# Performance work log

Measured on AMD Instinct MI355X. Metric: run time of the kernel, lower is better.

## Reference

```python
import jax, jax.numpy as jnp
import numpy as np

H = 1024  # hidden_size


def _lstm_layer(x, w_ih, w_hh, b_ih, b_hh):
    # x: [S, B, I] -> outputs [S, B, H]
    S, B, _ = x.shape
    # Precompute input projection for all timesteps (both biases folded in,
    # matching gi + gh where gi carries b_ih and gh carries b_hh).
    gi = jnp.einsum('sbi,gi->sbg', x, w_ih) + b_ih + b_hh  # [S, B, 4H]
    h0 = jnp.zeros((B, H), x.dtype)
    c0 = jnp.zeros((B, H), x.dtype)

    def step(carry, gi_t):
        h, c = carry
        gates = gi_t + h @ w_hh.T                # [B, 4H]
        i, f, g, o = jnp.split(gates, 4, axis=1)  # gate order: i, f, g, o
        c_new = jax.nn.sigmoid(f) * c + jax.nn.sigmoid(i) * jnp.tanh(g)
        h_new = jax.nn.sigmoid(o) * jnp.tanh(c_new)
        return (h_new, c_new), h_new

    (h_last, c_last), ys = jax.lax.scan(step, (h0, c0), gi)
    return ys, h_last, c_last


def setup_inputs() -> dict:
    key = jax.random.key(0)
    ks = jax.random.split(key, 6)
    S, B, I = 512, 64, 1024
    def xavier(k, shape):
        fan_out, fan_in = shape
        lim = np.sqrt(6.0 / (fan_in + fan_out)).astype(np.float32)
        return jax.random.uniform(k, shape, jnp.float32, -lim, lim)
    return {
        'x': jax.random.normal(ks[0], (S, B, I), jnp.float32),
        'w_ih_0': xavier(ks[1], (4 * H, I)),
        'w_hh_0': xavier(ks[2], (4 * H, H)),
        'b_ih_0': jnp.zeros((4 * H,), jnp.float32),
        'b_hh_0': jnp.zeros((4 * H,), jnp.float32),
        'w_ih_1': xavier(ks[3], (4 * H, H)),
        'w_hh_1': xavier(ks[4], (4 * H, H)),
        'b_ih_1': jnp.zeros((4 * H,), jnp.float32),
        'b_hh_1': jnp.zeros((4 * H,), jnp.float32),
    }


def reference(x, w_ih_0, w_hh_0, b_ih_0, b_hh_0, w_ih_1, w_hh_1, b_ih_1, b_hh_1):
    # 2-layer unidirectional LSTM, dropout=0, batch_first=False, zero init state.
    y0, h0, c0 = _lstm_layer(x, w_ih_0, w_hh_0, b_ih_0, b_hh_0)
    y1, h1, c1 = _lstm_layer(y0, w_ih_1, w_hh_1, b_ih_1, b_hh_1)
    h_n = jnp.stack([h0, h1], axis=0)  # [num_layers, B, H]
    c_n = jnp.stack([c0, c1], axis=0)
    return y1, h_n, c_n
```

## Files before the change

### kernel.cpp

```cpp
#include <hip/hip_runtime.h>

typedef __attribute__((ext_vector_type(8))) short short8;
typedef __attribute__((ext_vector_type(4))) float f32x4;
typedef unsigned int uint32;
typedef unsigned long long u64;

#define OFF_GI    0ull
#define OFF_XB    268435456ull
#define OFF_WIH0  335544320ull
#define OFF_WPKI  343932928ull
#define OFF_WPK0  352321536ull
#define OFF_WPK1  360710144ull
#define OFF_B0    369098752ull
#define OFF_B1    369115136ull
#define OFF_CNT   369131520ull
#define OFF_HBUF  369164288ull
#define WS_REQUIRED 369426432ull

#define ALOAD(p)    __hip_atomic_load((p), __ATOMIC_RELAXED, __HIP_MEMORY_SCOPE_AGENT)
#define ASTOREV(p,v) __hip_atomic_store((p), (v), __ATOMIC_RELAXED, __HIP_MEMORY_SCOPE_AGENT)
#define AADD(p,v)   __hip_atomic_fetch_add((p), (v), __ATOMIC_RELAXED, __HIP_MEMORY_SCOPE_AGENT)
#define WD_ITERS 30000

__device__ __forceinline__ unsigned short f2bf(float f) {
    union { float f; uint32 u; } v; v.f = f;
    uint32 u = v.u + 0x7FFFu + ((v.u >> 16) & 1u);
    return (unsigned short)(u >> 16);
}
__device__ __forceinline__ float bf2f(unsigned short u) {
    union { uint32 u; float f; } v; v.u = ((uint32)u) << 16; return v.f;
}
__device__ __forceinline__ float sigmoidf_(float x) {
    return 1.0f / (1.0f + __expf(-x));
}
__device__ __forceinline__ float tanhf_(float x) {
    return 1.0f - 2.0f / (1.0f + __expf(2.0f * x));
}

__global__ void diag_kernel(float* out, float val) {
    if (blockIdx.x == 0 && threadIdx.x == 0) out[0] = val;
}

__global__ void cast_bf16_kernel(const float* __restrict__ in,
                                 unsigned short* __restrict__ out, int n4) {
    int i = blockIdx.x * 256 + threadIdx.x;
    if (i < n4) {
        float4 v = ((const float4*)in)[i];
        ushort4 o;
        o.x = f2bf(v.x); o.y = f2bf(v.y); o.z = f2bf(v.z); o.w = f2bf(v.w);
        ((ushort4*)out)[i] = o;
    }
}

__global__ void bias_sum_kernel(const float* __restrict__ a,
                                const float* __restrict__ b,
                                float* __restrict__ o, int n) {
    int i = blockIdx.x * 256 + threadIdx.x;
    if (i < n) o[i] = a[i] + b[i];
}

__global__ void bias_perm_kernel(const float* __restrict__ a,
                                 const float* __restrict__ b,
                                 float* __restrict__ o) {
    int i = blockIdx.x * 256 + threadIdx.x;
    int c = i >> 2, g = i & 3;
    o[i] = a[g * 1024 + c] + b[g * 1024 + c];
}

__global__ void pack_whh_kernel(const float* __restrict__ whh,
                                unsigned short* __restrict__ out) {
    int o = blockIdx.x * 256 + threadIdx.x;
    int j  = o & 7;
    int l  = (o >> 3) & 63;
    int f  = (o >> 9) & 31;
    int wq = o >> 14;
    int w = wq >> 2, q = wq & 3;
    int g = f >> 3,  s = f & 7;
    int n = g * 1024 + w * 16 + (l & 15);
    int k = q * 256 + s * 32 + ((l >> 4)) * 8 + j;
    out[o] = f2bf(whh[(size_t)n * 1024 + k]);
}

__global__ void pack_wih1_frag_kernel(const float* __restrict__ wih1,
                                      unsigned short* __restrict__ out) {
    int o = blockIdx.x * 256 + threadIdx.x;
    int j  = o & 7;
    int l  = (o >> 3) & 63;
    int ks = (o >> 9) & 31;
    int wq = o >> 14;
    int w = wq >> 2, q = wq & 3;
    int np = w * 64 + q * 16 + (l & 15);
    int c = np >> 2, g = np & 3;
    int k = ks * 32 + ((l >> 4)) * 8 + j;
    out[o] = f2bf(wih1[(size_t)(g * 1024 + c) * 1024 + k]);
}

__global__ __launch_bounds__(256, 2) void gemm_bt_kernel(
    const unsigned short* __restrict__ A,
    const unsigned short* __restrict__ B,
    const float* __restrict__ bias,
    unsigned short* __restrict__ C) {
    __shared__ __align__(16) unsigned short As[128 * 64];
    __shared__ __align__(16) unsigned short Bs[128 * 64];
    const int tid = threadIdx.x;
    const int l = tid & 63;
    const int wv = tid >> 6;
    const int wm = wv >> 1, wn = wv & 1;
    const long bm = blockIdx.x, bn = blockIdx.y;

    f32x4 acc[4][4];
#pragma unroll
    for (int i = 0; i < 4; ++i)
#pragma unroll
        for (int j = 0; j < 4; ++j)
            acc[i][j] = (f32x4){0.f, 0.f, 0.f, 0.f};

    for (int k0 = 0; k0 < 1024; k0 += 64) {
#pragma unroll
        for (int ii = 0; ii < 4; ++ii) {
            int slot = ii * 256 + tid;
            int row = slot >> 3, csw = slot & 7;
            int cc = csw ^ (row & 7);
            *(uint4*)&As[slot * 8] =
                *(const uint4*)(A + (bm * 128 + row) * 1024 + k0 + cc * 8);
            *(uint4*)&Bs[slot * 8] =
                *(const uint4*)(B + (bn * 128 + row) * 1024 + k0 + cc * 8);
        }
        __syncthreads();
#pragma unroll
        for (int s = 0; s < 2; ++s) {
            short8 af[4], bfm[4];
#pragma unroll
            for (int i = 0; i < 4; ++i) {
                int row = wm * 64 + i * 16 + (l & 15);
                af[i] = *(const short8*)&As[(row * 8 + (((s * 4) + (l >> 4)) ^ (row & 7))) * 8];
            }
#pragma unroll
            for (int j = 0; j < 4; ++j) {
                int row = wn * 64 + j * 16 + (l & 15);
                bfm[j] = *(const short8*)&Bs[(row * 8 + (((s * 4) + (l >> 4)) ^ (row & 7))) * 8];
            }
#pragma unroll
            for (int i = 0; i < 4; ++i)
#pragma unroll
                for (int j = 0; j < 4; ++j)
                    acc[i][j] = __builtin_amdgcn_mfma_f32_16x16x32_bf16(
                        af[i], bfm[j], acc[i][j], 0, 0, 0);
        }
        __syncthreads();
    }
#pragma unroll
    for (int j = 0; j < 4; ++j) {
        float bj = bias[bn * 128 + wn * 64 + j * 16 + (l & 15)];
#pragma unroll
        for (int i = 0; i < 4; ++i) {
#pragma unroll
            for (int r = 0; r < 4; ++r) {
                long row = bm * 128 + wm * 64 + i * 16 + (l >> 4) * 4 + r;
                C[row * 4096 + bn * 128 + wn * 64 + j * 16 + (l & 15)] =
                    f2bf(acc[i][j][r] + bj);
            }
        }
    }
}

__device__ __forceinline__ void gi1_tile(
    const unsigned short* hs,
    const unsigned short* __restrict__ wpkI,
    const float* __restrict__ b1p,
    unsigned short* gi1,
    int tg, int p, int w, int q, int l)
{
    f32x4 gacc = (f32x4){0.f, 0.f, 0.f, 0.f};
    const int arow = l & 15;
    const unsigned short* wb = wpkI + (size_t)(w * 4 + q) * 16384 + (size_t)l * 8;
#pragma unroll 4
    for (int ks = 0; ks < 32; ++ks) {
        short8 bfk = *(const short8*)(wb + ks * 512);
        short8 afk = *(const short8*)&hs[(arow * 128 + ((ks * 4 + (l >> 4)) ^ (arow & 7))) * 8];
        gacc = __builtin_amdgcn_mfma_f32_16x16x32_bf16(afk, bfk, gacc, 0, 0, 0);
    }
    const int colp = w * 64 + q * 16 + (l & 15);
    float bj = b1p[colp];
#pragma unroll
    for (int r = 0; r < 4; ++r) {
        int v0 = f2bf(gacc[r] + bj);
        int v1 = __shfl_down(v0, 1);
        int v2 = __shfl_down(v0, 2);
        int v3 = __shfl_down(v0, 3);
        if ((l & 3) == 0) {
            size_t row = (size_t)tg * 64 + p * 16 + (l >> 4) * 4 + r;
            u64 u = (u64)(v0 & 0xffff) | ((u64)(v1 & 0xffff) << 16) |
                    ((u64)(v2 & 0xffff) << 32) | ((u64)(v3 & 0xffff) << 48);
            *(u64*)(gi1 + row * 4096 + colp) = u;
        }
    }
}

__global__ __launch_bounds__(256, 2) void lstm_l0_fused_kernel(
    unsigned short* gi,
    const unsigned short* __restrict__ wpk0,
    const unsigned short* __restrict__ wpkI,
    const float* __restrict__ b1p,
    unsigned short* hbuf,
    float* __restrict__ hn, float* __restrict__ cn,
    int* cnt)
{
    __shared__ __align__(16) char smem[49152];
    const int bid = blockIdx.x;
    const int tid = threadIdx.x;
    const int l = tid & 63, q = tid >> 6;

    if (bid < 256) {
        unsigned short* hs = (unsigned short*)smem;
        float (*red)[4][16][16] = (float (*)[4][16][16])(smem + 32768);
        const int p = bid >> 6, w = bid & 63;
        int* cg = cnt + p * 2048;
        int* pr = cnt + p * 2048 + 1024;

        short8 bfr[4][8];
        {
            const unsigned short* wb = wpk0 + (size_t)((w * 4 + q) * 32) * 512 + (size_t)l * 8;
#pragma unroll
            for (int g = 0; g < 4; ++g)
#pragma unroll
                for (int s = 0; s < 8; ++s)
                    bfr[g][s] = *(const short8*)(wb + (g * 8 + s) * 512);
        }

        float c_state = 0.0f;
        const int be = tid >> 4, je = tid & 15;
        const int hrow = p * 16 + be;
        const int hcol = w * 16 + je;

        for (int t = 0; t < 512; ++t) {
            const unsigned short* gp = gi + (size_t)t * 262144 + (size_t)hrow * 4096 + hcol;
            float g0 = bf2f(gp[0]);
            float g1 = bf2f(gp[1024]);
            float g2 = bf2f(gp[2048]);
            float g3 = bf2f(gp[3072]);

            if (tid == 0) {
                if (t > 0) {
                    int iters = 0;
                    while (ALOAD(&cg[t - 1]) < 64) {
                        __builtin_amdgcn_s_sleep(2);
                        if (++iters > WD_ITERS) break;
                    }
                }
                if (t >= 2) {
                    int iters = 0;
                    while (ALOAD(&pr[t - 2]) < 64) {
                        __builtin_amdgcn_s_sleep(2);
                        if (++iters > WD_ITERS) break;
                    }
                }
            }
            __syncthreads();

            {
                const u64* hp64 = (const u64*)(hbuf + (size_t)(t & 1) * 65536);
#pragma unroll
                for (int ii = 0; ii < 8; ++ii) {
                    int slot = ii * 256 + tid;
                    int row = slot >> 7, cs = slot & 127;
                    int cc = cs ^ (row & 7);
                    size_t gidx = ((size_t)(p * 16 + row) * 1024 + (size_t)cc * 8) >> 2;
                    u64 lo = ALOAD(&hp64[gidx]);
                    u64 hi = ALOAD(&hp64[gidx + 1]);
                    *(u64*)&hs[slot * 8]     = lo;
                    *(u64*)&hs[slot * 8 + 4] = hi;
                }
            }
            __syncthreads();

            f32x4 acc[4];
#pragma unroll
            for (int g = 0; g < 4; ++g) acc[g] = (f32x4){0.f, 0.f, 0.f, 0.f};
            const int arow = l & 15;
#pragma unroll
            for (int s = 0; s < 8; ++s) {
                int chunk = q * 32 + s * 4 + (l >> 4);
                short8 af = *(const short8*)&hs[(arow * 128 + (chunk ^ (arow & 7))) * 8];
#pragma unroll
                for (int g = 0; g < 4; ++g)
                    acc[g] = __builtin_amdgcn_mfma_f32_16x16x32_bf16(
                        af, bfr[g][s], acc[g], 0, 0, 0);
            }
#pragma unroll
            for (int g = 0; g < 4; ++g)
#pragma unroll
                for (int r = 0; r < 4; ++r)
                    red[q][g][(l >> 4) * 4 + r][l & 15] = acc[g][r];
            __syncthreads();

            float gate_i = g0, gate_f = g1, gate_g = g2, gate_o = g3;
#pragma unroll
            for (int qq = 0; qq < 4; ++qq) {
                gate_i += red[qq][0][be][je];
                gate_f += red[qq][1][be][je];
                gate_g += red[qq][2][be][je];
                gate_o += red[qq][3][be][je];
            }
            float ig = sigmoidf_(gate_i);
            float fg = sigmoidf_(gate_f);
            float gg = tanhf_(gate_g);
            float og = sigmoidf_(gate_o);
            c_state = fg * c_state + ig * gg;
            float h_new = og * tanhf_(c_state);

            unsigned short hb = f2bf(h_new);
            {
                int v0 = hb;
                int v1 = __shfl_down(v0, 1);
                int v2 = __shfl_down(v0, 2);
                int v3 = __shfl_down(v0, 3);
                if ((l & 3) == 0) {
                    u64 u = (u64)(v0 & 0xffff) | ((u64)(v1 & 0xffff) << 16) |
                            ((u64)(v2 & 0xffff) << 32) | ((u64)(v3 & 0xffff) << 48);
                    u64* dst = (u64*)(hbuf + (size_t)((t + 1) & 1) * 65536 +
                                      (size_t)hrow * 1024 + hcol);
                    ASTOREV(dst, u);
                }
            }
            if (t == 511) {
                hn[(size_t)hrow * 1024 + hcol] = h_new;
                cn[(size_t)hrow * 1024 + hcol] = c_state;
            }
            __syncthreads();
            if (tid == 0) AADD(&cg[t], 1);
        }
    } else {
        unsigned short* hs = (unsigned short*)smem;
        const int W = bid - 256;
        const int p = W >> 6, w = W & 63;
        int* cg = cnt + p * 2048;
        int* pr = cnt + p * 2048 + 1024;

        for (int t = 0; t < 512; ++t) {
            if (tid == 0) {
                int iters = 0;
                while (ALOAD(&cg[t]) < 64) {
                    __builtin_amdgcn_s_sleep(2);
                    if (++iters > WD_ITERS) break;
                }
            }
            __syncthreads();

            {
                const u64* hp64 = (const u64*)(hbuf + (size_t)((t + 1) & 1) * 65536);
#pragma unroll
                for (int ii = 0; ii < 8; ++ii) {
                    int slot = ii * 256 + tid;
                    int row = slot >> 7, cs = slot & 127;
                    int cc = cs ^ (row & 7);
                    size_t gidx = ((size_t)(p * 16 + row) * 1024 + (size_t)cc * 8) >> 2;
                    u64 lo = ALOAD(&hp64[gidx]);
                    u64 hi = ALOAD(&hp64[gidx + 1]);
                    *(u64*)&hs[slot * 8]     = lo;
                    *(u64*)&hs[slot * 8 + 4] = hi;
                }
            }
            __syncthreads();
            if (tid == 0) AADD(&pr[t], 1);

            gi1_tile(hs, wpkI, b1p, gi, t, p, w, q, l);
        }
    }
}

__global__ __launch_bounds__(256, 2) void lstm_rec1_kernel(
    const unsigned short* __restrict__ gi,
    const unsigned short* __restrict__ wpk,
    unsigned short* hbuf,
    float* __restrict__ yf,
    float* __restrict__ hn, float* __restrict__ cn,
    int* cnt) {
    __shared__ __align__(16) unsigned short hs[16 * 1024];
    __shared__ float red[4][4][16][16];
    const int tid = threadIdx.x;
    const int l = tid & 63, q = tid >> 6;
    const int W = blockIdx.x;
    const int p = W >> 6, w = W & 63;
    int* cg = cnt + p * 2048;

    short8 bfr[4][8];
    {
        const unsigned short* wb = wpk + (size_t)((w * 4 + q) * 32) * 512 + (size_t)l * 8;
#pragma unroll
        for (int g = 0; g < 4; ++g)
#pragma unroll
            for (int s = 0; s < 8; ++s)
                bfr[g][s] = *(const short8*)(wb + (g * 8 + s) * 512);
    }

    float c_state = 0.0f;
    const int be = tid >> 4, je = tid & 15;
    const int hrow = p * 16 + be;
    const int hcol = w * 16 + je;

    for (int t = 0; t < 512; ++t) {
        u64 gv = *(const u64*)(gi + ((size_t)t * 64 + hrow) * 4096 + (size_t)hcol * 4);
        float g0 = bf2f((unsigned short)gv);
        float g1 = bf2f((unsigned short)(gv >> 16));
        float g2 = bf2f((unsigned short)(gv >> 32));
        float g3 = bf2f((unsigned short)(gv >> 48));

        if (t > 0 && tid == 0) {
            int iters = 0;
            while (ALOAD(&cg[t - 1]) < 64) {
                __builtin_amdgcn_s_sleep(2);
                if (++iters > WD_ITERS) break;
            }
        }
        __syncthreads();

        {
            const u64* hp64 = (const u64*)(hbuf + (size_t)(t & 1) * 65536);
#pragma unroll
            for (int ii = 0; ii < 8; ++ii) {
                int slot = ii * 256 + tid;
                int row = slot >> 7, cs = slot & 127;
                int cc = cs ^ (row & 7);
                size_t gidx = ((size_t)(p * 16 + row) * 1024 + (size_t)cc * 8) >> 2;
                u64 lo = ALOAD(&hp64[gidx]);
                u64 hi = ALOAD(&hp64[gidx + 1]);
                *(u64*)&hs[slot * 8]     = lo;
                *(u64*)&hs[slot * 8 + 4] = hi;
            }
        }
        __syncthreads();

        f32x4 acc[4];
#pragma unroll
        for (int g = 0; g < 4; ++g) acc[g] = (f32x4){0.f, 0.f, 0.f, 0.f};
        const int arow = l & 15;
#pragma unroll
        for (int s = 0; s < 8; ++s) {
            int chunk = q * 32 + s * 4 + (l >> 4);
            short8 af = *(const short8*)&hs[(arow * 128 + (chunk ^ (arow & 7))) * 8];
#pragma unroll
            for (int g = 0; g < 4; ++g)
                acc[g] = __builtin_amdgcn_mfma_f32_16x16x32_bf16(
                    af, bfr[g][s], acc[g], 0, 0, 0);
        }
#pragma unroll
        for (int g = 0; g < 4; ++g)
#pragma unroll
            for (int r = 0; r < 4; ++r)
                red[q][g][(l >> 4) * 4 + r][l & 15] = acc[g][r];
        __syncthreads();

        float gate_i = g0, gate_f = g1, gate_g = g2, gate_o = g3;
#pragma unroll
        for (int qq = 0; qq < 4; ++qq) {
            gate_i += red[qq][0][be][je];
            gate_f += red[qq][1][be][je];
            gate_g += red[qq][2][be][je];
            gate_o += red[qq][3][be][je];
        }
        float ig = sigmoidf_(gate_i);
        float fg = sigmoidf_(gate_f);
        float gg = tanhf_(gate_g);
        float og = sigmoidf_(gate_o);
        c_state = fg * c_state + ig * gg;
        float h_new = og * tanhf_(c_state);

        unsigned short hb = f2bf(h_new);
        {
            int v0 = hb;
            int v1 = __shfl_down(v0, 1);
            int v2 = __shfl_down(v0, 2);
            int v3 = __shfl_down(v0, 3);
            if ((l & 3) == 0) {
                u64 u = (u64)(v0 & 0xffff) | ((u64)(v1 & 0xffff) << 16) |
                        ((u64)(v2 & 0xffff) << 32) | ((u64)(v3 & 0xffff) << 48);
                u64* dst = (u64*)(hbuf + (size_t)((t + 1) & 1) * 65536 +
                                  (size_t)hrow * 1024 + hcol);
                ASTOREV(dst, u);
            }
        }
        yf[(size_t)t * 65536 + (size_t)hrow * 1024 + hcol] = h_new;
        if (t == 511) {
            hn[(size_t)hrow * 1024 + hcol] = h_new;
            cn[(size_t)hrow * 1024 + hcol] = c_state;
        }
        __syncthreads();
        if (tid == 0) AADD(&cg[t], 1);
    }
}

extern "C" void kernel_launch(void* const* d_in, const int* in_sizes, int n_in,
                              void* d_out, int out_size, void* d_ws, size_t ws_size,
                              hipStream_t stream) {
    const float* x    = (const float*)d_in[0];
    const float* wih0 = (const float*)d_in[1];
    const float* whh0 = (const float*)d_in[2];
    const float* bih0 = (const float*)d_in[3];
    const float* bhh0 = (const float*)d_in[4];
    const float* wih1 = (const float*)d_in[5];
    const float* whh1 = (const float*)d_in[6];
    const float* bih1 = (const float*)d_in[7];
    const float* bhh1 = (const float*)d_in[8];
    float* out = (float*)d_out;

    if (ws_size < WS_REQUIRED) {
        diag_kernel<<<1, 64, 0, stream>>>(out, (float)(ws_size >> 20));
        return;
    }

    char* ws = (char*)d_ws;
    unsigned short* gi    = (unsigned short*)(ws + OFF_GI);
    unsigned short* xb    = (unsigned short*)(ws + OFF_XB);
    unsigned short* wih0b = (unsigned short*)(ws + OFF_WIH0);
    unsigned short* wpkI  = (unsigned short*)(ws + OFF_WPKI);
    unsigned short* wpk0  = (unsigned short*)(ws + OFF_WPK0);
    unsigned short* wpk1  = (unsigned short*)(ws + OFF_WPK1);
    float*          b0    = (float*)(ws + OFF_B0);
    float*          b1p   = (float*)(ws + OFF_B1);
    int*            cnt   = (int*)(ws + OFF_CNT);
    unsigned short* hbuf  = (unsigned short*)(ws + OFF_HBUF);

    cast_bf16_kernel<<<32768, 256, 0, stream>>>(x, xb, 8388608);
    cast_bf16_kernel<<<4096, 256, 0, stream>>>(wih0, wih0b, 1048576);
    pack_wih1_frag_kernel<<<16384, 256, 0, stream>>>(wih1, wpkI);
    pack_whh_kernel<<<16384, 256, 0, stream>>>(whh0, wpk0);
    pack_whh_kernel<<<16384, 256, 0, stream>>>(whh1, wpk1);
    bias_sum_kernel<<<16, 256, 0, stream>>>(bih0, bhh0, b0, 4096);
    bias_perm_kernel<<<16, 256, 0, stream>>>(bih1, bhh1, b1p);

    gemm_bt_kernel<<<dim3(256, 32), 256, 0, stream>>>(xb, wih0b, b0, gi);

    hipMemsetAsync(cnt, 0, 32768 + 262144, stream);
    lstm_l0_fused_kernel<<<512, 256, 0, stream>>>(gi, wpk0, wpkI, b1p, hbuf,
                                                  out + 33554432, out + 33685504,
                                                  cnt);
    hipMemsetAsync(cnt, 0, 32768 + 262144, stream);
    lstm_rec1_kernel<<<256, 256, 0, stream>>>(gi, wpk1, hbuf, out,
                                              out + 33554432 + 65536,
                                              out + 33685504 + 65536,
                                              cnt);
}
```

Measured before the change: 5.998 ms.

## Run both LSTM layers concurrently in one persistent kernel with wavefront pipelining

Merges the layer-0 recurrence, the layer-1 input projection and the layer-1 recurrence into a single persistent kernel. Blocks 0-255 run layer 0 while blocks 256-511 run layer 1 a few steps behind, exchanging h through an 8-slot ring buffer guarded by per-step counters. The x-to-bf16 cast is also folded into the GEMM's A-tile load, which removes a separate pass over x. This trades two serialized 512-step recurrences for one pipelined schedule, at the cost of more cross-block synchronization and more shared memory per block. Layer 1 now computes its input projection for step t+1 on its own critical path.

```diff
diff --git a/kernel.cpp b/kernel.cpp
--- a/kernel.cpp
+++ b/kernel.cpp
@@ -6,15 +6,15 @@
 typedef unsigned long long u64;
 
 #define OFF_GI    0ull
-#define OFF_XB    268435456ull
+#define OFF_Y0R   268435456ull
+#define OFF_H1B   269484032ull
+#define OFF_CNT2  269746176ull
 #define OFF_WIH0  335544320ull
 #define OFF_WPKI  343932928ull
 #define OFF_WPK0  352321536ull
 #define OFF_WPK1  360710144ull
 #define OFF_B0    369098752ull
 #define OFF_B1    369115136ull
-#define OFF_CNT   369131520ull
-#define OFF_HBUF  369164288ull
 #define WS_REQUIRED 369426432ull
 
 #define ALOAD(p)    __hip_atomic_load((p), __ATOMIC_RELAXED, __HIP_MEMORY_SCOPE_AGENT)
@@ -95,8 +95,8 @@
     out[o] = f2bf(wih1[(size_t)(g * 1024 + c) * 1024 + k]);
 }
 
-__global__ __launch_bounds__(256, 2) void gemm_bt_kernel(
-    const unsigned short* __restrict__ A,
+__global__ __launch_bounds__(256, 2) void gemm_bt_f32a_kernel(
+    const float* __restrict__ A,
     const unsigned short* __restrict__ B,
     const float* __restrict__ bias,
     unsigned short* __restrict__ C) {
@@ -121,8 +121,14 @@
             int slot = ii * 256 + tid;
             int row = slot >> 3, csw = slot & 7;
             int cc = csw ^ (row & 7);
-            *(uint4*)&As[slot * 8] =
-                *(const uint4*)(A + (bm * 128 + row) * 1024 + k0 + cc * 8);
+            const float* ap = A + (size_t)(bm * 128 + row) * 1024 + k0 + cc * 8;
+            float4 va = ((const float4*)ap)[0];
+            float4 vb = ((const float4*)ap)[1];
+            ushort4 ua, ub;
+            ua.x = f2bf(va.x); ua.y = f2bf(va.y); ua.z = f2bf(va.z); ua.w = f2bf(va.w);
+            ub.x = f2bf(vb.x); ub.y = f2bf(vb.y); ub.z = f2bf(vb.z); ub.w = f2bf(vb.w);
+            *(ushort4*)&As[slot * 8]     = ua;
+            *(ushort4*)&As[slot * 8 + 4] = ub;
             *(uint4*)&Bs[slot * 8] =
                 *(const uint4*)(B + (bn * 128 + row) * 1024 + k0 + cc * 8);
         }
@@ -164,60 +170,34 @@
     }
 }
 
-__device__ __forceinline__ void gi1_tile(
-    const unsigned short* hs,
+__global__ __launch_bounds__(256, 2) void lstm_fused2_kernel(
+    const unsigned short* __restrict__ gi0,
+    const unsigned short* __restrict__ wpk0,
+    const unsigned short* __restrict__ wpk1,
     const unsigned short* __restrict__ wpkI,
     const float* __restrict__ b1p,
-    unsigned short* gi1,
-    int tg, int p, int w, int q, int l)
-{
-    f32x4 gacc = (f32x4){0.f, 0.f, 0.f, 0.f};
-    const int arow = l & 15;
-    const unsigned short* wb = wpkI + (size_t)(w * 4 + q) * 16384 + (size_t)l * 8;
-#pragma unroll 4
-    for (int ks = 0; ks < 32; ++ks) {
-        short8 bfk = *(const short8*)(wb + ks * 512);
-        short8 afk = *(const short8*)&hs[(arow * 128 + ((ks * 4 + (l >> 4)) ^ (arow & 7))) * 8];
-        gacc = __builtin_amdgcn_mfma_f32_16x16x32_bf16(afk, bfk, gacc, 0, 0, 0);
-    }
-    const int colp = w * 64 + q * 16 + (l & 15);
-    float bj = b1p[colp];
-#pragma unroll
-    for (int r = 0; r < 4; ++r) {
-        int v0 = f2bf(gacc[r] + bj);
-        int v1 = __shfl_down(v0, 1);
-        int v2 = __shfl_down(v0, 2);
-        int v3 = __shfl_down(v0, 3);
-        if ((l & 3) == 0) {
-            size_t row = (size_t)tg * 64 + p * 16 + (l >> 4) * 4 + r;
-            u64 u = (u64)(v0 & 0xffff) | ((u64)(v1 & 0xffff) << 16) |
-                    ((u64)(v2 & 0xffff) << 32) | ((u64)(v3 & 0xffff) << 48);
-            *(u64*)(gi1 + row * 4096 + colp) = u;
-        }
-    }
-}
-
-__global__ __launch_bounds__(256, 2) void lstm_l0_fused_kernel(
-    unsigned short* gi,
-    const unsigned short* __restrict__ wpk0,
-    const unsigned short* __restrict__ wpkI,
-    const float* __restrict__ b1p,
-    unsigned short* hbuf,
-    float* __restrict__ hn, float* __restrict__ cn,
+    unsigned short* y0r,
+    unsigned short* h1b,
+    float* __restrict__ yf, float* __restrict__ hn, float* __restrict__ cn,
     int* cnt)
 {
-    __shared__ __align__(16) char smem[49152];
-    const int bid = blockIdx.x;
+    __shared__ __align__(16) char smem[53504];
+    unsigned short* hs = (unsigned short*)smem;
+    float (*red)[4][16][16] = (float (*)[4][16][16])(smem + 32768);
+    float* red2 = (float*)(smem + 49152);
     const int tid = threadIdx.x;
     const int l = tid & 63, q = tid >> 6;
-
-    if (bid < 256) {
-        unsigned short* hs = (unsigned short*)smem;
-        float (*red)[4][16][16] = (float (*)[4][16][16])(smem + 32768);
-        const int p = bid >> 6, w = bid & 63;
-        int* cg = cnt + p * 2048;
-        int* pr = cnt + p * 2048 + 1024;
-
+    const int bid = blockIdx.x;
+    const int role = bid >> 8;
+    const int W = bid & 255;
+    const int p = W >> 6, w = W & 63;
+    int* cg0 = cnt + p * 2048;
+    int* cg1 = cnt + p * 2048 + 1024;
+    const int be = tid >> 4, je = tid & 15;
+    const int hrow = p * 16 + be;
+    const int hcol = w * 16 + je;
+
+    if (role == 0) {
         short8 bfr[4][8];
         {
             const unsigned short* wb = wpk0 + (size_t)((w * 4 + q) * 32) * 512 + (size_t)l * 8;
@@ -227,14 +207,10 @@
                 for (int s = 0; s < 8; ++s)
                     bfr[g][s] = *(const short8*)(wb + (g * 8 + s) * 512);
         }
-
         float c_state = 0.0f;
-        const int be = tid >> 4, je = tid & 15;
-        const int hrow = p * 16 + be;
-        const int hcol = w * 16 + je;
 
         for (int t = 0; t < 512; ++t) {
-            const unsigned short* gp = gi + (size_t)t * 262144 + (size_t)hrow * 4096 + hcol;
+            const unsigned short* gp = gi0 + (size_t)t * 262144 + (size_t)hrow * 4096 + hcol;
             float g0 = bf2f(gp[0]);
             float g1 = bf2f(gp[1024]);
             float g2 = bf2f(gp[2048]);
@@ -243,14 +219,14 @@
             if (tid == 0) {
                 if (t > 0) {
                     int iters = 0;
-                    while (ALOAD(&cg[t - 1]) < 64) {
+                    while (ALOAD(&cg0[t - 1]) < 64) {
                         __builtin_amdgcn_s_sleep(2);
                         if (++iters > WD_ITERS) break;
                     }
                 }
-                if (t >= 2) {
+                if (t >= 8) {
                     int iters = 0;
-                    while (ALOAD(&pr[t - 2]) < 64) {
+                    while (ALOAD(&cg1[t - 8]) < 64) {
                         __builtin_amdgcn_s_sleep(2);
                         if (++iters > WD_ITERS) break;
                     }
@@ -259,7 +235,7 @@
             __syncthreads();
 
             {
-                const u64* hp64 = (const u64*)(hbuf + (size_t)(t & 1) * 65536);
+                const u64* hp64 = (const u64*)(y0r + (size_t)(t & 7) * 65536);
 #pragma unroll
                 for (int ii = 0; ii < 8; ++ii) {
                     int slot = ii * 256 + tid;
@@ -318,7 +294,7 @@
                 if ((l & 3) == 0) {
                     u64 u = (u64)(v0 & 0xffff) | ((u64)(v1 & 0xffff) << 16) |
                             ((u64)(v2 & 0xffff) << 32) | ((u64)(v3 & 0xffff) << 48);
-                    u64* dst = (u64*)(hbuf + (size_t)((t + 1) & 1) * 65536 +
+                    u64* dst = (u64*)(y0r + (size_t)((t + 1) & 7) * 65536 +
                                       (size_t)hrow * 1024 + hcol);
                     ASTOREV(dst, u);
                 }
@@ -328,19 +304,64 @@
                 cn[(size_t)hrow * 1024 + hcol] = c_state;
             }
             __syncthreads();
-            if (tid == 0) AADD(&cg[t], 1);
+            if (tid == 0) AADD(&cg0[t], 1);
         }
     } else {
-        unsigned short* hs = (unsigned short*)smem;
-        const int W = bid - 256;
-        const int p = W >> 6, w = W & 63;
-        int* cg = cnt + p * 2048;
-        int* pr = cnt + p * 2048 + 1024;
+        short8 bfr[4][8];
+        {
+            const unsigned short* wb = wpk1 + (size_t)((w * 4 + q) * 32) * 512 + (size_t)l * 8;
+#pragma unroll
+            for (int g = 0; g < 4; ++g)
+#pragma unroll
+                for (int s = 0; s < 8; ++s)
+                    bfr[g][s] = *(const short8*)(wb + (g * 8 + s) * 512);
+        }
+        const float4 bq = *(const float4*)&b1p[w * 64 + je * 4];
+        const unsigned short* wbI = wpkI + (size_t)(w * 4 + q) * 16384 + (size_t)l * 8;
+        float c_state = 0.0f;
+        const int arow = l & 15;
+
+        if (tid == 0) {
+            int iters = 0;
+            while (ALOAD(&cg0[0]) < 64) {
+                __builtin_amdgcn_s_sleep(2);
+                if (++iters > WD_ITERS) break;
+            }
+        }
+        __syncthreads();
+        {
+            const u64* hp64 = (const u64*)(y0r + (size_t)1 * 65536);
+#pragma unroll
+            for (int ii = 0; ii < 8; ++ii) {
+                int slot = ii * 256 + tid;
+                int row = slot >> 7, cs = slot & 127;
+                int cc = cs ^ (row & 7);
+                size_t gidx = ((size_t)(p * 16 + row) * 1024 + (size_t)cc * 8) >> 2;
+                u64 lo = ALOAD(&hp64[gidx]);
+                u64 hi = ALOAD(&hp64[gidx + 1]);
+                *(u64*)&hs[slot * 8]     = lo;
+                *(u64*)&hs[slot * 8 + 4] = hi;
+            }
+        }
+        __syncthreads();
+        {
+            f32x4 gacc = (f32x4){0.f, 0.f, 0.f, 0.f};
+#pragma unroll 4
+            for (int ks = 0; ks < 32; ++ks) {
+                short8 bfk = *(const short8*)(wbI + ks * 512);
+                short8 afk = *(const short8*)&hs[(arow * 128 + ((ks * 4 + (l >> 4)) ^ (arow & 7))) * 8];
+                gacc = __builtin_amdgcn_mfma_f32_16x16x32_bf16(afk, bfk, gacc, 0, 0, 0);
+            }
+#pragma unroll
+            for (int r = 0; r < 4; ++r)
+                red2[(q * 16 + (l & 15)) * 17 + (l >> 4) * 4 + r] = gacc[r];
+        }
+        __syncthreads();
 
         for (int t = 0; t < 512; ++t) {
-            if (tid == 0) {
+            if (t > 0 && tid == 0) {
                 int iters = 0;
-                while (ALOAD(&cg[t]) < 64) {
+                while (ALOAD(&cg1[t - 1]) < 64) {
                     __builtin_amdgcn_s_sleep(2);
                     if (++iters > WD_ITERS) break;
                 }
@@ -348,7 +369,7 @@
             __syncthreads();
 
             {
-                const u64* hp64 = (const u64*)(hbuf + (size_t)((t + 1) & 1) * 65536);
+                const u64* hp64 = (const u64*)(h1b + (size_t)(t & 1) * 65536);
 #pragma unroll
                 for (int ii = 0; ii < 8; ++ii) {
                     int slot = ii * 256 + tid;
@@ -362,131 +383,104 @@
                 }
             }
             __syncthreads();
-            if (tid == 0) AADD(&pr[t], 1);
-
-            gi1_tile(hs, wpkI, b1p, gi, t, p, w, q, l);
-        }
-    }
-}
-
-__global__ __launch_bounds__(256, 2) void lstm_rec1_kernel(
-    const unsigned short* __restrict__ gi,
-    const unsigned short* __restrict__ wpk,
-    unsigned short* hbuf,
-    float* __restrict__ yf,
-    float* __restrict__ hn, float* __restrict__ cn,
-    int* cnt) {
-    __shared__ __align__(16) unsigned short hs[16 * 1024];
-    __shared__ float red[4][4][16][16];
-    const int tid = threadIdx.x;
-    const int l = tid & 63, q = tid >> 6;
-    const int W = blockIdx.x;
-    const int p = W >> 6, w = W & 63;
-    int* cg = cnt + p * 2048;
-
-    short8 bfr[4][8];
-    {
-        const unsigned short* wb = wpk + (size_t)((w * 4 + q) * 32) * 512 + (size_t)l * 8;
-#pragma unroll
-        for (int g = 0; g < 4; ++g)
-#pragma unroll
-            for (int s = 0; s < 8; ++s)
-                bfr[g][s] = *(const short8*)(wb + (g * 8 + s) * 512);
-    }
-
-    float c_state = 0.0f;
-    const int be = tid >> 4, je = tid & 15;
-    const int hrow = p * 16 + be;
-    const int hcol = w * 16 + je;
-
-    for (int t = 0; t < 512; ++t) {
-        u64 gv = *(const u64*)(gi + ((size_t)t * 64 + hrow) * 4096 + (size_t)hcol * 4);
-        float g0 = bf2f((unsigned short)gv);
-        float g1 = bf2f((unsigned short)(gv >> 16));
-        float g2 = bf2f((unsigned short)(gv >> 32));
-        float g3 = bf2f((unsigned short)(gv >> 48));
-
-        if (t > 0 && tid == 0) {
-            int iters = 0;
-            while (ALOAD(&cg[t - 1]) < 64) {
-                __builtin_amdgcn_s_sleep(2);
-                if (++iters > WD_ITERS) break;
-            }
-        }
-        __syncthreads();
-
-        {
-            const u64* hp64 = (const u64*)(hbuf + (size_t)(t & 1) * 65536);
-#pragma unroll
-            for (int ii = 0; ii < 8; ++ii) {
-                int slot = ii * 256 + tid;
-                int row = slot >> 7, cs = slot & 127;
-                int cc = cs ^ (row & 7);
-                size_t gidx = ((size_t)(p * 16 + row) * 1024 + (size_t)cc * 8) >> 2;
-                u64 lo = ALOAD(&hp64[gidx]);
-                u64 hi = ALOAD(&hp64[gidx + 1]);
-                *(u64*)&hs[slot * 8]     = lo;
-                *(u64*)&hs[slot * 8 + 4] = hi;
-            }
-        }
-        __syncthreads();
-
-        f32x4 acc[4];
-#pragma unroll
-        for (int g = 0; g < 4; ++g) acc[g] = (f32x4){0.f, 0.f, 0.f, 0.f};
-        const int arow = l & 15;
-#pragma unroll
-        for (int s = 0; s < 8; ++s) {
-            int chunk = q * 32 + s * 4 + (l >> 4);
-            short8 af = *(const short8*)&hs[(arow * 128 + (chunk ^ (arow & 7))) * 8];
+
+            f32x4 acc[4];
+#pragma unroll
+            for (int g = 0; g < 4; ++g) acc[g] = (f32x4){0.f, 0.f, 0.f, 0.f};
+#pragma unroll
+            for (int s = 0; s < 8; ++s) {
+                int chunk = q * 32 + s * 4 + (l >> 4);
+                short8 af = *(const short8*)&hs[(arow * 128 + (chunk ^ (arow & 7))) * 8];
+#pragma unroll
+                for (int g = 0; g < 4; ++g)
+                    acc[g] = __builtin_amdgcn_mfma_f32_16x16x32_bf16(
+                        af, bfr[g][s], acc[g], 0, 0, 0);
+            }
 #pragma unroll
             for (int g = 0; g < 4; ++g)
-                acc[g] = __builtin_amdgcn_mfma_f32_16x16x32_bf16(
-                    af, bfr[g][s], acc[g], 0, 0, 0);
-        }
-#pragma unroll
-        for (int g = 0; g < 4; ++g)
-#pragma unroll
-            for (int r = 0; r < 4; ++r)
-                red[q][g][(l >> 4) * 4 + r][l & 15] = acc[g][r];
-        __syncthreads();
-
-        float gate_i = g0, gate_f = g1, gate_g = g2, gate_o = g3;
-#pragma unroll
-        for (int qq = 0; qq < 4; ++qq) {
-            gate_i += red[qq][0][be][je];
-            gate_f += red[qq][1][be][je];
-            gate_g += red[qq][2][be][je];
-            gate_o += red[qq][3][be][je];
-        }
-        float ig = sigmoidf_(gate_i);
-        float fg = sigmoidf_(gate_f);
-        float gg = tanhf_(gate_g);
-        float og = sigmoidf_(gate_o);
-        c_state = fg * c_state + ig * gg;
-        float h_new = og * tanhf_(c_state);
-
-        unsigned short hb = f2bf(h_new);
-        {
-            int v0 = hb;
-            int v1 = __shfl_down(v0, 1);
-            int v2 = __shfl_down(v0, 2);
-            int v3 = __shfl_down(v0, 3);
-            if ((l & 3) == 0) {
-                u64 u = (u64)(v0 & 0xffff) | ((u64)(v1 & 0xffff) << 16) |
-                        ((u64)(v2 & 0xffff) << 32) | ((u64)(v3 & 0xffff) << 48);
-                u64* dst = (u64*)(hbuf + (size_t)((t + 1) & 1) * 65536 +
-                                  (size_t)hrow * 1024 + hcol);
-                ASTOREV(dst, u);
-            }
-        }
-        yf[(size_t)t * 65536 + (size_t)hrow * 1024 + hcol] = h_new;
-        if (t == 511) {
-            hn[(size_t)hrow * 1024 + hcol] = h_new;
-            cn[(size_t)hrow * 1024 + hcol] = c_state;
-        }
-        __syncthreads();
-        if (tid == 0) AADD(&cg[t], 1);
+#pragma unroll
+                for (int r = 0; r < 4; ++r)
+                    red[q][g][(l >> 4) * 4 + r][l & 15] = acc[g][r];
+            __syncthreads();
+
+            float gate_i = red2[(je * 4 + 0) * 17 + be] + bq.x;
+            float gate_f = red2[(je * 4 + 1) * 17 + be] + bq.y;
+            float gate_g = red2[(je * 4 + 2) * 17 + be] + bq.z;
+            float gate_o = red2[(je * 4 + 3) * 17 + be] + bq.w;
+#pragma unroll
+            for (int qq = 0; qq < 4; ++qq) {
+                gate_i += red[qq][0][be][je];
+                gate_f += red[qq][1][be][je];
+                gate_g += red[qq][2][be][je];
+                gate_o += red[qq][3][be][je];
+            }
+            float ig = sigmoidf_(gate_i);
+            float fg = sigmoidf_(gate_f);
+            float gg = tanhf_(gate_g);
+            float og = sigmoidf_(gate_o);
+            c_state = fg * c_state + ig * gg;
+            float h_new = og * tanhf_(c_state);
+
+            unsigned short hb = f2bf(h_new);
+            {
+                int v0 = hb;
+                int v1 = __shfl_down(v0, 1);
+                int v2 = __shfl_down(v0, 2);
+                int v3 = __shfl_down(v0, 3);
+                if ((l & 3) == 0) {
+                    u64 u = (u64)(v0 & 0xffff) | ((u64)(v1 & 0xffff) << 16) |
+                            ((u64)(v2 & 0xffff) << 32) | ((u64)(v3 & 0xffff) << 48);
+                    u64* dst = (u64*)(h1b + (size_t)((t + 1) & 1) * 65536 +
+                                      (size_t)hrow * 1024 + hcol);
+                    ASTOREV(dst, u);
+                }
+            }
+            yf[(size_t)t * 65536 + (size_t)hrow * 1024 + hcol] = h_new;
+            if (t == 511) {
+                hn[65536 + (size_t)hrow * 1024 + hcol] = h_new;
+                cn[65536 + (size_t)hrow * 1024 + hcol] = c_state;
+            }
+            __syncthreads();
+            if (tid == 0) AADD(&cg1[t], 1);
+
+            if (t < 511) {
+                if (tid == 0) {
+                    int iters = 0;
+                    while (ALOAD(&cg0[t + 1]) < 64) {
+                        __builtin_amdgcn_s_sleep(2);
+                        if (++iters > WD_ITERS) break;
+                    }
+                }
+                __syncthreads();
+                {
+                    const u64* hp64 = (const u64*)(y0r + (size_t)((t + 2) & 7) * 65536);
+#pragma unroll
+                    for (int ii = 0; ii < 8; ++ii) {
+                        int slot = ii * 256 + tid;
+                        int row = slot >> 7, cs = slot & 127;
+                        int cc = cs ^ (row & 7);
+                        size_t gidx = ((size_t)(p * 16 + row) * 1024 + (size_t)cc * 8) >> 2;
+                        u64 lo = ALOAD(&hp64[gidx]);
+                        u64 hi = ALOAD(&hp64[gidx + 1]);
+                        *(u64*)&hs[slot * 8]     = lo;
+                        *(u64*)&hs[slot * 8 + 4] = hi;
+                    }
+                }
+                __syncthreads();
+                {
+                    f32x4 gacc = (f32x4){0.f, 0.f, 0.f, 0.f};
+#pragma unroll 4
+                    for (int ks = 0; ks < 32; ++ks) {
+                        short8 bfk = *(const short8*)(wbI + ks * 512);
+                        short8 afk = *(const short8*)&hs[(arow * 128 + ((ks * 4 + (l >> 4)) ^ (arow & 7))) * 8];
+                        gacc = __builtin_amdgcn_mfma_f32_16x16x32_bf16(afk, bfk, gacc, 0, 0, 0);
+                    }
+#pragma unroll
+                    for (int r = 0; r < 4; ++r)
+                        red2[(q * 16 + (l & 15)) * 17 + (l >> 4) * 4 + r] = gacc[r];
+                }
+            }
+        }
     }
 }
 
@@ -511,17 +505,18 @@
 
     char* ws = (char*)d_ws;
     unsigned short* gi    = (unsigned short*)(ws + OFF_GI);
-    unsigned short* xb    = (unsigned short*)(ws + OFF_XB);
+    unsigned short* y0r   = (unsigned short*)(ws + OFF_Y0R);
+    unsigned short* h1b   = (unsigned short*)(ws + OFF_H1B);
+    int*            cnt   = (int*)(ws + OFF_CNT2);
     unsigned short* wih0b = (unsigned short*)(ws + OFF_WIH0);
     unsigned short* wpkI  = (unsigned short*)(ws + OFF_WPKI);
     unsigned short* wpk0  = (unsigned short*)(ws + OFF_WPK0);
     unsigned short* wpk1  = (unsigned short*)(ws + OFF_WPK1);
     float*          b0    = (float*)(ws + OFF_B0);
     float*          b1p   = (float*)(ws + OFF_B1);
-    int*            cnt   = (int*)(ws + OFF_CNT);
-    unsigned short* hbuf  = (unsigned short*)(ws + OFF_HBUF);
-
-    cast_bf16_kernel<<<32768, 256, 0, stream>>>(x, xb, 8388608);
+
+    hipMemsetAsync(ws + OFF_Y0R, 0, 1343488, stream);
+
     cast_bf16_kernel<<<4096, 256, 0, stream>>>(wih0, wih0b, 1048576);
     pack_wih1_frag_kernel<<<16384, 256, 0, stream>>>(wih1, wpkI);
     pack_whh_kernel<<<16384, 256, 0, stream>>>(whh0, wpk0);
@@ -529,15 +524,10 @@
     bias_sum_kernel<<<16, 256, 0, stream>>>(bih0, bhh0, b0, 4096);
     bias_perm_kernel<<<16, 256, 0, stream>>>(bih1, bhh1, b1p);
 
-    gemm_bt_kernel<<<dim3(256, 32), 256, 0, stream>>>(xb, wih0b, b0, gi);
-
-    hipMemsetAsync(cnt, 0, 32768 + 262144, stream);
-    lstm_l0_fused_kernel<<<512, 256, 0, stream>>>(gi, wpk0, wpkI, b1p, hbuf,
-                                                  out + 33554432, out + 33685504,
-                                                  cnt);
-    hipMemsetAsync(cnt, 0, 32768 + 262144, stream);
-    lstm_rec1_kernel<<<256, 256, 0, stream>>>(gi, wpk1, hbuf, out,
-                                              out + 33554432 + 65536,
-                                              out + 33685504 + 65536,
-                                              cnt);
-}
+    gemm_bt_f32a_kernel<<<dim3(256, 32), 256, 0, stream>>>(x, wih0b, b0, gi);
+
+    lstm_fused2_kernel<<<512, 256, 0, stream>>>(gi, wpk0, wpk1, wpkI, b1p,
+                                                y0r, h1b,
+                                                out, out + 33554432, out + 33685504,
+                                                cnt);
+}
```

Result: faster. 5.484 ms (-8.6%).
